# Optimization experiments

Measured on AMD Instinct MI355X. Metric: run time of the kernel, lower is better.

## Reference

```python
import jax, jax.numpy as jnp
import numpy as np

N_NODES = 10000
N_EDGES = 70000
IN_DIM = 10
HEADS = 6
LIN_OUT = 254
GAT_DIMS = [(256, 508), (512, 250), (256, 120), (128, 20)]  # (in_dim, out_dim) per DeformGAT
NEG_SLOPE = 0.2


def setup_inputs() -> dict:
    key = jax.random.key(0)
    ks = jax.random.split(key, 8)
    inp = {}
    inp["data"] = jax.random.normal(ks[0], (N_NODES, IN_DIM), dtype=jnp.float32)
    inp["edge_idx"] = jax.random.randint(ks[1], (2, N_EDGES), 0, N_NODES)
    inp["bd_mask"] = jax.random.randint(ks[2], (N_NODES,), 0, 2) > 0
    inp["poly_mesh"] = 0
    inp["W_lin"] = jax.random.normal(ks[3], (IN_DIM, LIN_OUT), dtype=jnp.float32) * 0.05
    inp["b_lin"] = jnp.zeros((LIN_OUT,), dtype=jnp.float32)
    for i, (din, dout) in enumerate(GAT_DIMS):
        k1, k2, k3 = jax.random.split(ks[4 + i], 3)
        inp[f"W{i+1}"] = jax.random.normal(k1, (din, HEADS * dout), dtype=jnp.float32) * 0.05
        inp[f"asrc{i+1}"] = jax.random.normal(k2, (HEADS, dout), dtype=jnp.float32) * 0.05
        inp[f"adst{i+1}"] = jax.random.normal(k3, (HEADS, dout), dtype=jnp.float32) * 0.05
    return inp


def deform_gat(coord, feat, src, dst, bd_mask, W, a_src, a_dst, n):
    """One DeformGAT layer: GAT attention over edge list; features aggregated
    (head-averaged, SELU); coords moved to attention-weighted neighbor centroid,
    boundary nodes pinned."""
    H, C = a_src.shape
    x = (feat @ W).reshape(-1, H, C)                       # [N,H,C]
    a_s = jnp.einsum('nhc,hc->nh', x, a_src)               # [N,H]
    a_d = jnp.einsum('nhc,hc->nh', x, a_dst)               # [N,H]
    e = jax.nn.leaky_relu(a_s[src] + a_d[dst], NEG_SLOPE)  # [E,H]
    # segment softmax over incoming edges of each dst node
    m = jax.ops.segment_max(e, dst, num_segments=n)
    m = jnp.where(jnp.isfinite(m), m, 0.0)
    ex = jnp.exp(e - m[dst])
    denom = jax.ops.segment_sum(ex, dst, num_segments=n)
    alpha = ex / jnp.where(denom[dst] > 0, denom[dst], 1.0)        # [E,H]
    agg = jax.ops.segment_sum(alpha[:, :, None] * x[src], dst, num_segments=n)  # [N,H,C]
    out_feat = jax.nn.selu(agg.mean(axis=1))                       # [N,C]
    am = alpha.mean(axis=1)                                        # [E]
    new_coord = jax.ops.segment_sum(am[:, None] * coord[src], dst, num_segments=n)  # [N,2]
    out_coord = jnp.where(bd_mask[:, None], coord, new_coord)
    return out_coord, out_feat


def reference(data, edge_idx, bd_mask, poly_mesh, W_lin, b_lin,
              W1, asrc1, adst1, W2, asrc2, adst2,
              W3, asrc3, adst3, W4, asrc4, adst4):
    n = data.shape[0]
    coords = data[:, 0:2]
    src, dst = edge_idx[0], edge_idx[1]
    h = jax.nn.selu(data @ W_lin + b_lin)                  # [N,254]
    t1 = jnp.concatenate([coords, h], axis=1)              # [N,256]
    c1, f1 = deform_gat(coords, t1, src, dst, bd_mask, W1, asrc1, adst1, n)
    t2 = jnp.concatenate([c1, coords, f1], axis=1)         # [N,512]
    c2, f2 = deform_gat(c1, t2, src, dst, bd_mask, W2, asrc2, adst2, n)
    t3 = jnp.concatenate([c2, c1, coords, f2], axis=1)     # [N,256]
    c3, f3 = deform_gat(c2, t3, src, dst, bd_mask, W3, asrc3, adst3, n)
    t4 = jnp.concatenate([c3, c2, c1, coords, f3], axis=1) # [N,128]
    c4, f4 = deform_gat(c3, t4, src, dst, bd_mask, W4, asrc4, adst4, n)
    return c4
```

## Files before the change

kernel.cpp:

```cpp
#include <hip/hip_runtime.h>
#include <hip/hip_bf16.h>

#define N_NODES 10000
#define N_EDGES 70000
#define HEADS 6
#define MPAD 10112
#define SELU_SCALE 1.0507009873554805f
#define SELU_ALPHA  1.6732632423543772f
#define NEG_SLOPE 0.2f

typedef __attribute__((ext_vector_type(8))) __bf16 bf16x8;
typedef __attribute__((ext_vector_type(4))) float f32x4;

__device__ __forceinline__ float selu_f(float x) {
    return x > 0.f ? SELU_SCALE * x : SELU_SCALE * SELU_ALPHA * (__expf(x) - 1.f);
}
__device__ __forceinline__ unsigned short f2bf(float f) {
    __hip_bfloat16 h = __float2bfloat16(f);
    return __builtin_bit_cast(unsigned short, h);
}
__device__ __forceinline__ float bf2f(unsigned short u) {
    unsigned int x = ((unsigned int)u) << 16;
    return __builtin_bit_cast(float, x);
}

__global__ void count_edges_k(const int* __restrict__ dstv, int* __restrict__ counts) {
    int e = blockIdx.x * blockDim.x + threadIdx.x;
    if (e < N_EDGES) atomicAdd(&counts[dstv[e]], 1);
}

__global__ __launch_bounds__(1024) void scan_k(const int* __restrict__ counts, int* __restrict__ offs) {
    __shared__ int part[1024];
    int tid = threadIdx.x;
    const int per = (N_NODES + 1023) / 1024;
    int start = tid * per;
    int s = 0;
    for (int i = 0; i < per; ++i) { int idx = start + i; if (idx < N_NODES) s += counts[idx]; }
    part[tid] = s;
    __syncthreads();
    for (int off = 1; off < 1024; off <<= 1) {
        int v = (tid >= off) ? part[tid - off] : 0;
        __syncthreads();
        part[tid] += v;
        __syncthreads();
    }
    int run = part[tid] - s;
    for (int i = 0; i < per; ++i) {
        int idx = start + i;
        if (idx < N_NODES) { offs[idx] = run; run += counts[idx]; }
    }
    if (tid == 0) offs[N_NODES] = part[1023];
}

__global__ void fill_csr_k(const int* __restrict__ dstv, const int* __restrict__ offs,
                           int* __restrict__ cursor, int* __restrict__ csr) {
    int e = blockIdx.x * blockDim.x + threadIdx.x;
    if (e < N_EDGES) {
        int d = dstv[e];
        int pos = atomicAdd(&cursor[d], 1);
        csr[offs[d] + pos] = e;
    }
}

__global__ __launch_bounds__(256) void prep_k(const float* __restrict__ data,
                                              const float* __restrict__ W,
                                              const float* __restrict__ b,
                                              float* __restrict__ coords0,
                                              unsigned short* __restrict__ t1) {
    int idx = blockIdx.x * blockDim.x + threadIdx.x;
    if (idx >= N_NODES * 256) return;
    int n = idx >> 8, c = idx & 255;
    if (c < 2) {
        float v = data[n * 10 + c];
        t1[(size_t)n * 256 + c] = f2bf(v);
        if (c == 0) {
            coords0[2 * n] = data[n * 10];
            coords0[2 * n + 1] = data[n * 10 + 1];
        }
    } else {
        int cc = c - 2;
        float acc = b[cc];
        const float* dr = data + (size_t)n * 10;
#pragma unroll
        for (int k = 0; k < 10; ++k) acc += dr[k] * W[k * 254 + cc];
        t1[(size_t)n * 256 + c] = f2bf(selu_f(acc));
    }
}

__global__ __launch_bounds__(64) void fold_all_k(
    const float* __restrict__ W0, const float* __restrict__ s0v, const float* __restrict__ d0v,
    const float* __restrict__ W1, const float* __restrict__ s1v, const float* __restrict__ d1v,
    const float* __restrict__ W2, const float* __restrict__ s2v, const float* __restrict__ d2v,
    const float* __restrict__ W3, const float* __restrict__ s3v, const float* __restrict__ d3v,
    float* __restrict__ wsf0, float* __restrict__ wdf0,
    float* __restrict__ wsf1, float* __restrict__ wdf1,
    float* __restrict__ wsf2, float* __restrict__ wdf2,
    float* __restrict__ wsf3, float* __restrict__ wdf3) {
    int bid = blockIdx.x;
    const float* W; const float* sv; const float* dv; float* ws; float* wd;
    int K, C, pair;
    if (bid < 1536)      { W = W0; sv = s0v; dv = d0v; ws = wsf0; wd = wdf0; K = 256; C = 508; pair = bid; }
    else if (bid < 4608) { W = W1; sv = s1v; dv = d1v; ws = wsf1; wd = wdf1; K = 512; C = 250; pair = bid - 1536; }
    else if (bid < 6144) { W = W2; sv = s2v; dv = d2v; ws = wsf2; wd = wdf2; K = 256; C = 120; pair = bid - 4608; }
    else                 { W = W3; sv = s3v; dv = d3v; ws = wsf3; wd = wdf3; K = 128; C = 20;  pair = bid - 6144; }
    int k = pair / HEADS, h = pair % HEADS;
    int lane = threadIdx.x;
    const float* wr = W + (size_t)k * (HEADS * C) + h * C;
    const float* sr = sv + h * C;
    const float* dr = dv + h * C;
    float s = 0.f, d = 0.f;
    for (int c = lane; c < C; c += 64) {
        float w = wr[c];
        s += w * sr[c];
        d += w * dr[c];
    }
#pragma unroll
    for (int off = 32; off > 0; off >>= 1) {
        s += __shfl_xor(s, off);
        d += __shfl_xor(d, off);
    }
    if (lane == 0) { ws[pair] = s; wd[pair] = d; }
}

__global__ __launch_bounds__(256) void convv_all_k(
    const float* __restrict__ W0, unsigned short* __restrict__ Vt0,
    const float* __restrict__ W1, unsigned short* __restrict__ Vt1,
    const float* __restrict__ W2, unsigned short* __restrict__ Vt2) {
    __shared__ float tile[64][65];
    int bid = blockIdx.x;
    const float* W; unsigned short* Vt; int K, C, K6, bid2, ktiles;
    if (bid < 192)      { W = W0; Vt = Vt0; K = 256; C = 508; K6 = 1536; bid2 = bid;       ktiles = 24; }
    else if (bid < 384) { W = W1; Vt = Vt1; K = 512; C = 250; K6 = 3072; bid2 = bid - 192; ktiles = 48; }
    else                { W = W2; Vt = Vt2; K = 256; C = 120; K6 = 1536; bid2 = bid - 384; ktiles = 24; }
    int kb = bid2 % ktiles, cb = bid2 / ktiles;
    const int tx = threadIdx.x;
    const int ty = threadIdx.y;
    const int k0 = kb * 64;
    const int c0 = cb * 64;
    for (int i = ty; i < 64; i += 4) {
        int kk = k0 + i;
        int h = kk / K, k = kk - h * K;
        int c = c0 + tx;
        tile[i][tx] = (c < C) ? W[(size_t)k * (HEADS * C) + h * C + c] : 0.f;
    }
    __syncthreads();
    for (int i = ty; i < 64; i += 4) {
        int c = c0 + i;
        Vt[(size_t)c * K6 + k0 + tx] = f2bf(tile[tx][i]);
    }
}

__global__ __launch_bounds__(256) void gemm_split_k(
    const unsigned short* __restrict__ A,
    const unsigned short* __restrict__ Bt,
    unsigned short* __restrict__ part,
    int Kpitch, int klen, int Npad) {
    __shared__ unsigned short lds[16384];
    const int tid = threadIdx.x;
    const int lane = tid & 63, wid = tid >> 6;
    const int wm = wid >> 1, wn = wid & 1;
    const int m0 = blockIdx.y * 128;
    const int n0 = blockIdx.x * 128;
    const int kz = blockIdx.z;
    const int kbeg = kz * klen;

    f32x4 acc[4][4] = {};

    const unsigned short* gsrc[8];
    unsigned ldsoff[8];
#pragma unroll
    for (int i = 0; i < 8; ++i) {
        const int half = i >> 2;
        const int slot = (i & 3) * 256 + tid;
        const int r = slot >> 3;
        const int c16 = slot & 7;
        const int ksl = c16 ^ (r & 7);
        gsrc[i] = (half ? (Bt + (size_t)(n0 + r) * Kpitch) : (A + (size_t)(m0 + r) * Kpitch)) + ksl * 8;
        ldsoff[i] = (unsigned)(half * 8192 + ((i & 3) * 256 + wid * 64) * 8);
    }

    for (int kt = kbeg; kt < kbeg + klen; kt += 64) {
#pragma unroll
        for (int i = 0; i < 8; ++i) {
            __builtin_amdgcn_global_load_lds(
                (const __attribute__((address_space(1))) unsigned int*)(gsrc[i] + kt),
                (__attribute__((address_space(3))) unsigned int*)(&lds[ldsoff[i]]),
                16, 0, 0);
        }
        __syncthreads();
#pragma unroll
        for (int kc = 0; kc < 2; ++kc) {
            const int xo = (((kc * 4 + (lane >> 4)) ^ (lane & 7)) << 4);
            bf16x8 aop[4], bop[4];
#pragma unroll
            for (int f = 0; f < 4; ++f) {
                const int rA = wm * 64 + f * 16 + (lane & 15);
                bop[f] = *(const bf16x8*)((const char*)lds + rA * 128 + xo);
                const int rB = wn * 64 + f * 16 + (lane & 15);
                aop[f] = *(const bf16x8*)((const char*)lds + 16384 * 1 + rB * 128 + xo);
            }
#pragma unroll
            for (int fm = 0; fm < 4; ++fm)
#pragma unroll
                for (int fn = 0; fn < 4; ++fn)
                    acc[fm][fn] = __builtin_amdgcn_mfma_f32_16x16x32_bf16(
                        aop[fn], bop[fm], acc[fm][fn], 0, 0, 0);
        }
        __syncthreads();
    }

    unsigned short* pbase = part + (size_t)kz * MPAD * Npad;
    const int mrow = m0 + wm * 64 + (lane & 15);
    const int ncol = n0 + wn * 64 + ((lane >> 4) * 4);
#pragma unroll
    for (int fm = 0; fm < 4; ++fm) {
#pragma unroll
        for (int fn = 0; fn < 4; ++fn) {
            f32x4 v = acc[fm][fn];
            unsigned int u0 = (unsigned int)f2bf(v.x) | ((unsigned int)f2bf(v.y) << 16);
            unsigned int u1 = (unsigned int)f2bf(v.z) | ((unsigned int)f2bf(v.w) << 16);
            uint2 pk = make_uint2(u0, u1);
            *(uint2*)&pbase[(size_t)(mrow + fm * 16) * Npad + ncol + fn * 16] = pk;
        }
    }
}

__global__ __launch_bounds__(256) void proj2_k(const unsigned short* __restrict__ t,
                                               const float* __restrict__ wsf,
                                               const float* __restrict__ wdf,
                                               float* __restrict__ a_s,
                                               float* __restrict__ a_d, int K) {
    const int wv = threadIdx.x >> 6;
    const int lane = threadIdx.x & 63;
    const int n = blockIdx.x * 4 + wv;
    if (n >= N_NODES) return;
    const unsigned short* tr = t + (size_t)n * K;
    const int kpl = K >> 6;
    const int k0 = lane * kpl;

    unsigned int buf[4] = {0u, 0u, 0u, 0u};
    if (kpl == 8) {
        uint4 u = *(const uint4*)(tr + k0);
        buf[0] = u.x; buf[1] = u.y; buf[2] = u.z; buf[3] = u.w;
    } else if (kpl == 4) {
        uint2 u = *(const uint2*)(tr + k0);
        buf[0] = u.x; buf[1] = u.y;
    } else {
        buf[0] = *(const unsigned int*)(tr + k0);
    }

    float s[HEADS] = {}, d[HEADS] = {};
#pragma unroll
    for (int j = 0; j < 8; ++j) {
        if (j >= kpl) break;
        unsigned int w = buf[j >> 1];
        unsigned short u = (j & 1) ? (unsigned short)(w >> 16) : (unsigned short)(w & 0xffff);
        float v = bf2f(u);
        const float* ws = wsf + (size_t)(k0 + j) * HEADS;
        const float* wd = wdf + (size_t)(k0 + j) * HEADS;
#pragma unroll
        for (int h = 0; h < HEADS; ++h) {
            s[h] += v * ws[h];
            d[h] += v * wd[h];
        }
    }
#pragma unroll
    for (int off = 32; off > 0; off >>= 1) {
#pragma unroll
        for (int h = 0; h < HEADS; ++h) {
            s[h] += __shfl_xor(s[h], off);
            d[h] += __shfl_xor(d[h], off);
        }
    }
    if (lane == 0) {
#pragma unroll
        for (int h = 0; h < HEADS; ++h) {
            a_s[n * HEADS + h] = s[h];
            a_d[n * HEADS + h] = d[h];
        }
    }
}

template<int KN>
__global__ __launch_bounds__(256) void reduceproj_k(
    const unsigned short* __restrict__ part, int KS, int Npad, int off,
    unsigned short* __restrict__ tnext,
    const float* __restrict__ wsf, const float* __restrict__ wdf,
    float* __restrict__ a_s, float* __restrict__ a_d) {
    const int wid = threadIdx.x >> 6, lane = threadIdx.x & 63;
    const int n = blockIdx.x * 4 + wid;
    if (n >= N_NODES) return;
    constexpr int KPL = KN / 64;
    const int c0 = lane * KPL;
    unsigned short* row = tnext + (size_t)n * KN;

    float vals[KPL];
#pragma unroll
    for (int q = 0; q < KPL; ++q) {
        int c = c0 + q;
        if (c < off) {
            vals[q] = bf2f(row[c]);
        } else {
            int cp = c - off;
            float sum = 0.f;
            for (int kz = 0; kz < KS; ++kz)
                sum += bf2f(part[(size_t)kz * MPAD * Npad + (size_t)n * Npad + cp]);
            float o = selu_f(sum * (1.f / 6.f));
            vals[q] = o;
            row[c] = f2bf(o);
        }
    }

    float s[HEADS] = {}, d[HEADS] = {};
#pragma unroll
    for (int q = 0; q < KPL; ++q) {
        int c = c0 + q;
        float v = vals[q];
        const float* ws = wsf + (size_t)c * HEADS;
        const float* wd = wdf + (size_t)c * HEADS;
#pragma unroll
        for (int h = 0; h < HEADS; ++h) {
            s[h] += v * ws[h];
            d[h] += v * wd[h];
        }
    }
#pragma unroll
    for (int off2 = 32; off2 > 0; off2 >>= 1) {
#pragma unroll
        for (int h = 0; h < HEADS; ++h) {
            s[h] += __shfl_xor(s[h], off2);
            d[h] += __shfl_xor(d[h], off2);
        }
    }
    if (lane == 0) {
#pragma unroll
        for (int h = 0; h < HEADS; ++h) {
            a_s[n * HEADS + h] = s[h];
            a_d[n * HEADS + h] = d[h];
        }
    }
}

template<int KT>
__global__ __launch_bounds__(256) void attn_agg_move_k(
    const float* __restrict__ a_s, const float* __restrict__ a_d,
    const int* __restrict__ srcv, const int* __restrict__ csr,
    const int* __restrict__ offs,
    const unsigned short* __restrict__ t_in, unsigned short* __restrict__ thagg,
    const float* __restrict__ cprev, const int* __restrict__ bd,
    float* __restrict__ cout, unsigned short* __restrict__ tnext, int ld,
    const float* __restrict__ xA, int offA,
    const float* __restrict__ xB, int offB) {
    const int wid = threadIdx.x >> 6, lane = threadIdx.x & 63;
    const int n = blockIdx.x * 4 + wid;
    if (n >= N_NODES) return;
    const int r0 = offs[n], r1 = offs[n + 1];

    float ad[HEADS], mm[HEADS], ss[HEADS];
#pragma unroll
    for (int h = 0; h < HEADS; ++h) {
        ad[h] = a_d[n * HEADS + h];
        mm[h] = -1e30f; ss[h] = 0.f;
    }

    for (int base = r0; base < r1; base += 64) {
        int i = base + lane;
        if (i < r1) {
            int src = srcv[csr[i]];
#pragma unroll
            for (int h = 0; h < HEADS; ++h) {
                float v = a_s[src * HEADS + h] + ad[h];
                v = v > 0.f ? v : NEG_SLOPE * v;
                float nm = fmaxf(mm[h], v);
                ss[h] = ss[h] * __expf(mm[h] - nm) + __expf(v - nm);
                mm[h] = nm;
            }
        }
    }
#pragma unroll
    for (int off = 32; off > 0; off >>= 1) {
#pragma unroll
        for (int h = 0; h < HEADS; ++h) {
            float mo = __shfl_xor(mm[h], off);
            float so = __shfl_xor(ss[h], off);
            float nm = fmaxf(mm[h], mo);
            ss[h] = ss[h] * __expf(mm[h] - nm) + so * __expf(mo - nm);
            mm[h] = nm;
        }
    }
    float rd[HEADS];
#pragma unroll
    for (int h = 0; h < HEADS; ++h) rd[h] = ss[h] > 0.f ? 1.f / ss[h] : 0.f;

    constexpr int KPL = (KT > 0) ? (KT / 64) : 1;
    float acc[HEADS][KPL] = {};
    float cx = 0.f, cy = 0.f;
    for (int base = r0; base < r1; base += 64) {
        int i = base + lane;
        bool ok = i < r1;
        int mysrc = ok ? srcv[csr[i]] : 0;
        float myal[HEADS];
#pragma unroll
        for (int h = 0; h < HEADS; ++h) myal[h] = 0.f;
        if (ok) {
            float am = 0.f;
#pragma unroll
            for (int h = 0; h < HEADS; ++h) {
                float v = a_s[mysrc * HEADS + h] + ad[h];
                v = v > 0.f ? v : NEG_SLOPE * v;
                float a = __expf(v - mm[h]) * rd[h];
                myal[h] = a;
                am += a;
            }
            am *= (1.f / 6.f);
            cx += am * cprev[2 * mysrc];
            cy += am * cprev[2 * mysrc + 1];
        }
        if constexpr (KT > 0) {
            int cnt = min(64, r1 - base);
            for (int j = 0; j < cnt; ++j) {
                int src = __shfl(mysrc, j);
                float al[HEADS];
#pragma unroll
                for (int h = 0; h < HEADS; ++h) al[h] = __shfl(myal[h], j);
                if constexpr (KT == 512) {
                    uint4 u = *(const uint4*)(t_in + (size_t)src * 512 + lane * 8);
                    float tv[8];
                    tv[0] = bf2f((unsigned short)(u.x & 0xffff)); tv[1] = bf2f((unsigned short)(u.x >> 16));
                    tv[2] = bf2f((unsigned short)(u.y & 0xffff)); tv[3] = bf2f((unsigned short)(u.y >> 16));
                    tv[4] = bf2f((unsigned short)(u.z & 0xffff)); tv[5] = bf2f((unsigned short)(u.z >> 16));
                    tv[6] = bf2f((unsigned short)(u.w & 0xffff)); tv[7] = bf2f((unsigned short)(u.w >> 16));
#pragma unroll
                    for (int h = 0; h < HEADS; ++h)
#pragma unroll
                        for (int q = 0; q < 8; ++q) acc[h][q] += al[h] * tv[q];
                } else {
                    uint2 u = *(const uint2*)(t_in + (size_t)src * 256 + lane * 4);
                    float tv[4];
                    tv[0] = bf2f((unsigned short)(u.x & 0xffff)); tv[1] = bf2f((unsigned short)(u.x >> 16));
                    tv[2] = bf2f((unsigned short)(u.y & 0xffff)); tv[3] = bf2f((unsigned short)(u.y >> 16));
#pragma unroll
                    for (int h = 0; h < HEADS; ++h)
#pragma unroll
                        for (int q = 0; q < 4; ++q) acc[h][q] += al[h] * tv[q];
                }
            }
        }
    }

    if constexpr (KT == 512) {
#pragma unroll
        for (int h = 0; h < HEADS; ++h) {
            uint4 pk;
            pk.x = (unsigned int)f2bf(acc[h][0]) | ((unsigned int)f2bf(acc[h][1]) << 16);
            pk.y = (unsigned int)f2bf(acc[h][2]) | ((unsigned int)f2bf(acc[h][3]) << 16);
            pk.z = (unsigned int)f2bf(acc[h][4]) | ((unsigned int)f2bf(acc[h][5]) << 16);
            pk.w = (unsigned int)f2bf(acc[h][6]) | ((unsigned int)f2bf(acc[h][7]) << 16);
            *(uint4*)(thagg + (size_t)n * 3072 + h * 512 + lane * 8) = pk;
        }
    } else if constexpr (KT == 256) {
#pragma unroll
        for (int h = 0; h < HEADS; ++h) {
            uint2 pk;
            pk.x = (unsigned int)f2bf(acc[h][0]) | ((unsigned int)f2bf(acc[h][1]) << 16);
            pk.y = (unsigned int)f2bf(acc[h][2]) | ((unsigned int)f2bf(acc[h][3]) << 16);
            *(uint2*)(thagg + (size_t)n * 1536 + h * 256 + lane * 4) = pk;
        }
    }
#pragma unroll
    for (int off = 32; off > 0; off >>= 1) {
        cx += __shfl_xor(cx, off);
        cy += __shfl_xor(cy, off);
    }
    if (lane == 0) {
        float px = cprev[2 * n], py = cprev[2 * n + 1];
        float ocx, ocy;
        if (bd[n] != 0) { ocx = px; ocy = py; }
        else { ocx = cx; ocy = cy; }
        cout[2 * n] = ocx; cout[2 * n + 1] = ocy;
        if (tnext) {
            unsigned short* row = tnext + (size_t)n * ld;
            row[0] = f2bf(ocx); row[1] = f2bf(ocy);
            row[2] = f2bf(px);  row[3] = f2bf(py);
            if (xA) { row[offA] = f2bf(xA[2 * n]); row[offA + 1] = f2bf(xA[2 * n + 1]); }
            if (xB) { row[offB] = f2bf(xB[2 * n]); row[offB + 1] = f2bf(xB[2 * n + 1]); }
        }
    }
}

static inline int cdiv(int a, int b) { return (a + b - 1) / b; }

extern "C" void kernel_launch(void* const* d_in, const int* in_sizes, int n_in,
                              void* d_out, int out_size, void* d_ws, size_t ws_size,
                              hipStream_t stream) {
    const float* data = (const float*)d_in[0];
    const int* eidx = (const int*)d_in[1];
    const int* bd = (const int*)d_in[2];
    const float* W_lin = (const float*)d_in[4];
    const float* b_lin = (const float*)d_in[5];
    const float* Wl[4]  = {(const float*)d_in[6],  (const float*)d_in[9],
                           (const float*)d_in[12], (const float*)d_in[15]};
    const float* Asrc[4] = {(const float*)d_in[7],  (const float*)d_in[10],
                            (const float*)d_in[13], (const float*)d_in[16]};
    const float* Adst[4] = {(const float*)d_in[8],  (const float*)d_in[11],
                            (const float*)d_in[14], (const float*)d_in[17]};
    const int Kd[4] = {256, 512, 256, 128};
    const int Cpadd[4] = {512, 256, 128, 0};
    const int KSd[4] = {2, 4, 4, 0};

    const int* srcv = eidx;
    const int* dstv = eidx + N_EDGES;

    char* p = (char*)d_ws;
    auto alloc = [&](size_t bytes) -> void* {
        void* r = (void*)p;
        p += (bytes + 255) & ~(size_t)255;
        return r;
    };
    unsigned short* tb1 = (unsigned short*)alloc((size_t)MPAD * 256 * 2);
    unsigned short* tb2 = (unsigned short*)alloc((size_t)MPAD * 512 * 2);
    unsigned short* tb3 = (unsigned short*)alloc((size_t)MPAD * 256 * 2);
    unsigned short* tb4 = (unsigned short*)alloc((size_t)MPAD * 128 * 2);
    unsigned short* thagg = (unsigned short*)alloc((size_t)MPAD * 3072 * 2);
    unsigned short* VtL[3];
    VtL[0] = (unsigned short*)alloc((size_t)512 * 1536 * 2);
    VtL[1] = (unsigned short*)alloc((size_t)256 * 3072 * 2);
    VtL[2] = (unsigned short*)alloc((size_t)128 * 1536 * 2);
    unsigned short* partb = (unsigned short*)alloc((size_t)8 * MPAD * 256 * 2);
    float* coords0 = (float*)alloc((size_t)N_NODES * 2 * 4);
    float* c1 = (float*)alloc((size_t)N_NODES * 2 * 4);
    float* c2 = (float*)alloc((size_t)N_NODES * 2 * 4);
    float* c3 = (float*)alloc((size_t)N_NODES * 2 * 4);
    float* a_s = (float*)alloc((size_t)N_NODES * HEADS * 4);
    float* a_d = (float*)alloc((size_t)N_NODES * HEADS * 4);
    float* wsfL[4]; float* wdfL[4];
    wsfL[0] = (float*)alloc(1536 * 4); wdfL[0] = (float*)alloc(1536 * 4);
    wsfL[1] = (float*)alloc(3072 * 4); wdfL[1] = (float*)alloc(3072 * 4);
    wsfL[2] = (float*)alloc(1536 * 4); wdfL[2] = (float*)alloc(1536 * 4);
    wsfL[3] = (float*)alloc(768 * 4);  wdfL[3] = (float*)alloc(768 * 4);
    int* counts = (int*)alloc((size_t)N_NODES * 4);
    int* cursor = (int*)alloc((size_t)N_NODES * 4);
    int* offs = (int*)alloc((size_t)(N_NODES + 1) * 4);
    int* csr = (int*)alloc((size_t)N_EDGES * 4);

    hipMemsetAsync(counts, 0, (size_t)((char*)offs - (char*)counts), stream);
    count_edges_k<<<cdiv(N_EDGES, 256), 256, 0, stream>>>(dstv, counts);
    scan_k<<<1, 1024, 0, stream>>>(counts, offs);
    fill_csr_k<<<cdiv(N_EDGES, 256), 256, 0, stream>>>(dstv, offs, cursor, csr);

    prep_k<<<cdiv(N_NODES * 256, 256), 256, 0, stream>>>(data, W_lin, b_lin, coords0, tb1);
    fold_all_k<<<6912, 64, 0, stream>>>(
        Wl[0], Asrc[0], Adst[0], Wl[1], Asrc[1], Adst[1],
        Wl[2], Asrc[2], Adst[2], Wl[3], Asrc[3], Adst[3],
        wsfL[0], wdfL[0], wsfL[1], wdfL[1], wsfL[2], wdfL[2], wsfL[3], wdfL[3]);
    convv_all_k<<<432, dim3(64, 4), 0, stream>>>(Wl[0], VtL[0], Wl[1], VtL[1], Wl[2], VtL[2]);

    unsigned short* tin[4]   = {tb1, tb2, tb3, tb4};
    unsigned short* tnext[4] = {tb2, tb3, tb4, nullptr};
    int ldn[4]  = {512, 256, 128, 0};
    int foff[4] = {4, 6, 8, 0};
    float* cprev[4] = {coords0, c1, c2, c3};
    float* cout[4]  = {c1, c2, c3, (float*)d_out};
    const float* xAv[4] = {nullptr, coords0, c1, nullptr};
    int offAv[4] = {0, 4, 4, 0};
    const float* xBv[4] = {nullptr, nullptr, coords0, nullptr};
    int offBv[4] = {0, 0, 6, 0};

    proj2_k<<<cdiv(N_NODES, 4), 256, 0, stream>>>(tb1, wsfL[0], wdfL[0], a_s, a_d, 256);

    for (int l = 0; l < 4; ++l) {
        int K = Kd[l], Cpad = Cpadd[l], KS = KSd[l];
        int K6 = K * HEADS;

        if (l == 3) {
            attn_agg_move_k<0><<<cdiv(N_NODES, 4), 256, 0, stream>>>(
                a_s, a_d, srcv, csr, offs, tin[l], nullptr,
                cprev[l], bd, cout[l], tnext[l], ldn[l],
                xAv[l], offAv[l], xBv[l], offBv[l]);
        } else if (K == 512) {
            attn_agg_move_k<512><<<cdiv(N_NODES, 4), 256, 0, stream>>>(
                a_s, a_d, srcv, csr, offs, tin[l], thagg,
                cprev[l], bd, cout[l], tnext[l], ldn[l],
                xAv[l], offAv[l], xBv[l], offBv[l]);
        } else {
            attn_agg_move_k<256><<<cdiv(N_NODES, 4), 256, 0, stream>>>(
                a_s, a_d, srcv, csr, offs, tin[l], thagg,
                cprev[l], bd, cout[l], tnext[l], ldn[l],
                xAv[l], offAv[l], xBv[l], offBv[l]);
        }

        if (l < 3) {
            int klen = K6 / KS;
            gemm_split_k<<<dim3(Cpad / 128, MPAD / 128, KS), 256, 0, stream>>>(
                thagg, VtL[l], partb, K6, klen, Cpad);
            if (ldn[l] == 512) {
                reduceproj_k<512><<<cdiv(N_NODES, 4), 256, 0, stream>>>(
                    partb, KS, Cpad, foff[l], tnext[l], wsfL[l + 1], wdfL[l + 1], a_s, a_d);
            } else if (ldn[l] == 256) {
                reduceproj_k<256><<<cdiv(N_NODES, 4), 256, 0, stream>>>(
                    partb, KS, Cpad, foff[l], tnext[l], wsfL[l + 1], wdfL[l + 1], a_s, a_d);
            } else {
                reduceproj_k<128><<<cdiv(N_NODES, 4), 256, 0, stream>>>(
                    partb, KS, Cpad, foff[l], tnext[l], wsfL[l + 1], wdfL[l + 1], a_s, a_d);
            }
        }
    }
}
```

Baseline: 331.1 us.

## Store source ids in CSR, fuse prep with projection, add single-pass softmax path

The CSR fill now stores source node ids directly, which removes one level of indirection (srcv[csr[i]]) in every attention kernel. The input linear+SELU prep is fused with the layer-1 attention projection into one wave-per-node kernel, dropping a separate launch and the re-read of t1. For nodes with degree at most 64, the attention kernel computes max, exp and sum in registers with wave reductions instead of an online-softmax loop followed by a second recompute pass. This adds code size and a divergent branch, and keeps the old two-pass path for high-degree nodes.

Measured after the change: 341.3 us. +3.1%, slower.

```diff
diff --git a/kernel.cpp b/kernel.cpp
--- a/kernel.cpp
+++ b/kernel.cpp
@@ -52,38 +52,77 @@
     if (tid == 0) offs[N_NODES] = part[1023];
 }
 
-__global__ void fill_csr_k(const int* __restrict__ dstv, const int* __restrict__ offs,
-                           int* __restrict__ cursor, int* __restrict__ csr) {
+__global__ void fill_csr_k(const int* __restrict__ srcv, const int* __restrict__ dstv,
+                           const int* __restrict__ offs,
+                           int* __restrict__ cursor, int* __restrict__ srcs) {
     int e = blockIdx.x * blockDim.x + threadIdx.x;
     if (e < N_EDGES) {
         int d = dstv[e];
         int pos = atomicAdd(&cursor[d], 1);
-        csr[offs[d] + pos] = e;
-    }
-}
-
-__global__ __launch_bounds__(256) void prep_k(const float* __restrict__ data,
-                                              const float* __restrict__ W,
-                                              const float* __restrict__ b,
-                                              float* __restrict__ coords0,
-                                              unsigned short* __restrict__ t1) {
-    int idx = blockIdx.x * blockDim.x + threadIdx.x;
-    if (idx >= N_NODES * 256) return;
-    int n = idx >> 8, c = idx & 255;
-    if (c < 2) {
-        float v = data[n * 10 + c];
-        t1[(size_t)n * 256 + c] = f2bf(v);
-        if (c == 0) {
-            coords0[2 * n] = data[n * 10];
-            coords0[2 * n + 1] = data[n * 10 + 1];
-        }
-    } else {
-        int cc = c - 2;
-        float acc = b[cc];
-        const float* dr = data + (size_t)n * 10;
-#pragma unroll
-        for (int k = 0; k < 10; ++k) acc += dr[k] * W[k * 254 + cc];
-        t1[(size_t)n * 256 + c] = f2bf(selu_f(acc));
+        srcs[offs[d] + pos] = srcv[e];
+    }
+}
+
+__global__ __launch_bounds__(256) void prep_proj_k(
+    const float* __restrict__ data, const float* __restrict__ W, const float* __restrict__ b,
+    float* __restrict__ coords0, unsigned short* __restrict__ t1,
+    const float* __restrict__ wsf, const float* __restrict__ wdf,
+    float* __restrict__ a_s, float* __restrict__ a_d) {
+    const int wid = threadIdx.x >> 6, lane = threadIdx.x & 63;
+    const int n = blockIdx.x * 4 + wid;
+    if (n >= N_NODES) return;
+    const int c0 = lane * 4;
+    const float* dr = data + (size_t)n * 10;
+
+    float vals[4];
+#pragma unroll
+    for (int q = 0; q < 4; ++q) {
+        int c = c0 + q;
+        if (c < 2) {
+            vals[q] = dr[c];
+        } else {
+            int cc = c - 2;
+            float acc = b[cc];
+#pragma unroll
+            for (int k = 0; k < 10; ++k) acc += dr[k] * W[k * 254 + cc];
+            vals[q] = selu_f(acc);
+        }
+    }
+    uint2 pk;
+    pk.x = (unsigned int)f2bf(vals[0]) | ((unsigned int)f2bf(vals[1]) << 16);
+    pk.y = (unsigned int)f2bf(vals[2]) | ((unsigned int)f2bf(vals[3]) << 16);
+    *(uint2*)(t1 + (size_t)n * 256 + c0) = pk;
+    if (lane == 0) {
+        coords0[2 * n] = vals[0];
+        coords0[2 * n + 1] = vals[1];
+    }
+
+    float s[HEADS] = {}, d[HEADS] = {};
+#pragma unroll
+    for (int q = 0; q < 4; ++q) {
+        float v = bf2f(f2bf(vals[q]));
+        const float* ws = wsf + (size_t)(c0 + q) * HEADS;
+        const float* wd = wdf + (size_t)(c0 + q) * HEADS;
+#pragma unroll
+        for (int h = 0; h < HEADS; ++h) {
+            s[h] += v * ws[h];
+            d[h] += v * wd[h];
+        }
+    }
+#pragma unroll
+    for (int off = 32; off > 0; off >>= 1) {
+#pragma unroll
+        for (int h = 0; h < HEADS; ++h) {
+            s[h] += __shfl_xor(s[h], off);
+            d[h] += __shfl_xor(d[h], off);
+        }
+    }
+    if (lane == 0) {
+#pragma unroll
+        for (int h = 0; h < HEADS; ++h) {
+            a_s[n * HEADS + h] = s[h];
+            a_d[n * HEADS + h] = d[h];
+        }
     }
 }
 
@@ -225,62 +264,6 @@
     }
 }
 
-__global__ __launch_bounds__(256) void proj2_k(const unsigned short* __restrict__ t,
-                                               const float* __restrict__ wsf,
-                                               const float* __restrict__ wdf,
-                                               float* __restrict__ a_s,
-                                               float* __restrict__ a_d, int K) {
-    const int wv = threadIdx.x >> 6;
-    const int lane = threadIdx.x & 63;
-    const int n = blockIdx.x * 4 + wv;
-    if (n >= N_NODES) return;
-    const unsigned short* tr = t + (size_t)n * K;
-    const int kpl = K >> 6;
-    const int k0 = lane * kpl;
-
-    unsigned int buf[4] = {0u, 0u, 0u, 0u};
-    if (kpl == 8) {
-        uint4 u = *(const uint4*)(tr + k0);
-        buf[0] = u.x; buf[1] = u.y; buf[2] = u.z; buf[3] = u.w;
-    } else if (kpl == 4) {
-        uint2 u = *(const uint2*)(tr + k0);
-        buf[0] = u.x; buf[1] = u.y;
-    } else {
-        buf[0] = *(const unsigned int*)(tr + k0);
-    }
-
-    float s[HEADS] = {}, d[HEADS] = {};
-#pragma unroll
-    for (int j = 0; j < 8; ++j) {
-        if (j >= kpl) break;
-        unsigned int w = buf[j >> 1];
-        unsigned short u = (j & 1) ? (unsigned short)(w >> 16) : (unsigned short)(w & 0xffff);
-        float v = bf2f(u);
-        const float* ws = wsf + (size_t)(k0 + j) * HEADS;
-        const float* wd = wdf + (size_t)(k0 + j) * HEADS;
-#pragma unroll
-        for (int h = 0; h < HEADS; ++h) {
-            s[h] += v * ws[h];
-            d[h] += v * wd[h];
-        }
-    }
-#pragma unroll
-    for (int off = 32; off > 0; off >>= 1) {
-#pragma unroll
-        for (int h = 0; h < HEADS; ++h) {
-            s[h] += __shfl_xor(s[h], off);
-            d[h] += __shfl_xor(d[h], off);
-        }
-    }
-    if (lane == 0) {
-#pragma unroll
-        for (int h = 0; h < HEADS; ++h) {
-            a_s[n * HEADS + h] = s[h];
-            a_d[n * HEADS + h] = d[h];
-        }
-    }
-}
-
 template<int KN>
 __global__ __launch_bounds__(256) void reduceproj_k(
     const unsigned short* __restrict__ part, int KS, int Npad, int off,
@@ -344,8 +327,7 @@
 template<int KT>
 __global__ __launch_bounds__(256) void attn_agg_move_k(
     const float* __restrict__ a_s, const float* __restrict__ a_d,
-    const int* __restrict__ srcv, const int* __restrict__ csr,
-    const int* __restrict__ offs,
+    const int* __restrict__ srcs, const int* __restrict__ offs,
     const unsigned short* __restrict__ t_in, unsigned short* __restrict__ thagg,
     const float* __restrict__ cprev, const int* __restrict__ bd,
     float* __restrict__ cout, unsigned short* __restrict__ tnext, int ld,
@@ -355,70 +337,61 @@
     const int n = blockIdx.x * 4 + wid;
     if (n >= N_NODES) return;
     const int r0 = offs[n], r1 = offs[n + 1];
-
-    float ad[HEADS], mm[HEADS], ss[HEADS];
-#pragma unroll
-    for (int h = 0; h < HEADS; ++h) {
-        ad[h] = a_d[n * HEADS + h];
-        mm[h] = -1e30f; ss[h] = 0.f;
-    }
-
-    for (int base = r0; base < r1; base += 64) {
-        int i = base + lane;
-        if (i < r1) {
-            int src = srcv[csr[i]];
-#pragma unroll
-            for (int h = 0; h < HEADS; ++h) {
-                float v = a_s[src * HEADS + h] + ad[h];
-                v = v > 0.f ? v : NEG_SLOPE * v;
-                float nm = fmaxf(mm[h], v);
-                ss[h] = ss[h] * __expf(mm[h] - nm) + __expf(v - nm);
-                mm[h] = nm;
-            }
-        }
-    }
-#pragma unroll
-    for (int off = 32; off > 0; off >>= 1) {
-#pragma unroll
-        for (int h = 0; h < HEADS; ++h) {
-            float mo = __shfl_xor(mm[h], off);
-            float so = __shfl_xor(ss[h], off);
-            float nm = fmaxf(mm[h], mo);
-            ss[h] = ss[h] * __expf(mm[h] - nm) + so * __expf(mo - nm);
-            mm[h] = nm;
-        }
-    }
-    float rd[HEADS];
-#pragma unroll
-    for (int h = 0; h < HEADS; ++h) rd[h] = ss[h] > 0.f ? 1.f / ss[h] : 0.f;
+    const int deg = r1 - r0;
+
+    float ad[HEADS];
+#pragma unroll
+    for (int h = 0; h < HEADS; ++h) ad[h] = a_d[n * HEADS + h];
 
     constexpr int KPL = (KT > 0) ? (KT / 64) : 1;
     float acc[HEADS][KPL] = {};
     float cx = 0.f, cy = 0.f;
-    for (int base = r0; base < r1; base += 64) {
-        int i = base + lane;
-        bool ok = i < r1;
-        int mysrc = ok ? srcv[csr[i]] : 0;
-        float myal[HEADS];
-#pragma unroll
-        for (int h = 0; h < HEADS; ++h) myal[h] = 0.f;
+
+    if (deg <= 64) {
+        const bool ok = lane < deg;
+        const int mysrc = ok ? srcs[r0 + lane] : 0;
+        float mm[HEADS], ss[HEADS], myal[HEADS];
+#pragma unroll
+        for (int h = 0; h < HEADS; ++h) {
+            float v = -1e30f;
+            if (ok) {
+                v = a_s[mysrc * HEADS + h] + ad[h];
+                v = v > 0.f ? v : NEG_SLOPE * v;
+            }
+            mm[h] = v;
+        }
+#pragma unroll
+        for (int off = 32; off > 0; off >>= 1)
+#pragma unroll
+            for (int h = 0; h < HEADS; ++h) mm[h] = fmaxf(mm[h], __shfl_xor(mm[h], off));
+#pragma unroll
+        for (int h = 0; h < HEADS; ++h) {
+            float v = -1e30f;
+            if (ok) {
+                v = a_s[mysrc * HEADS + h] + ad[h];
+                v = v > 0.f ? v : NEG_SLOPE * v;
+            }
+            myal[h] = ok ? __expf(v - mm[h]) : 0.f;
+            ss[h] = myal[h];
+        }
+#pragma unroll
+        for (int off = 32; off > 0; off >>= 1)
+#pragma unroll
+            for (int h = 0; h < HEADS; ++h) ss[h] += __shfl_xor(ss[h], off);
+        float am = 0.f;
+#pragma unroll
+        for (int h = 0; h < HEADS; ++h) {
+            float rdh = ss[h] > 0.f ? 1.f / ss[h] : 0.f;
+            myal[h] *= rdh;
+            am += myal[h];
+        }
         if (ok) {
-            float am = 0.f;
-#pragma unroll
-            for (int h = 0; h < HEADS; ++h) {
-                float v = a_s[mysrc * HEADS + h] + ad[h];
-                v = v > 0.f ? v : NEG_SLOPE * v;
-                float a = __expf(v - mm[h]) * rd[h];
-                myal[h] = a;
-                am += a;
-            }
             am *= (1.f / 6.f);
-            cx += am * cprev[2 * mysrc];
-            cy += am * cprev[2 * mysrc + 1];
+            cx = am * cprev[2 * mysrc];
+            cy = am * cprev[2 * mysrc + 1];
         }
         if constexpr (KT > 0) {
-            int cnt = min(64, r1 - base);
-            for (int j = 0; j < cnt; ++j) {
+            for (int j = 0; j < deg; ++j) {
                 int src = __shfl(mysrc, j);
                 float al[HEADS];
 #pragma unroll
@@ -443,6 +416,91 @@
                     for (int h = 0; h < HEADS; ++h)
 #pragma unroll
                         for (int q = 0; q < 4; ++q) acc[h][q] += al[h] * tv[q];
+                }
+            }
+        }
+    } else {
+        float mm[HEADS], ss[HEADS];
+#pragma unroll
+        for (int h = 0; h < HEADS; ++h) { mm[h] = -1e30f; ss[h] = 0.f; }
+        for (int base = r0; base < r1; base += 64) {
+            int i = base + lane;
+            if (i < r1) {
+                int src = srcs[i];
+#pragma unroll
+                for (int h = 0; h < HEADS; ++h) {
+                    float v = a_s[src * HEADS + h] + ad[h];
+                    v = v > 0.f ? v : NEG_SLOPE * v;
+                    float nm = fmaxf(mm[h], v);
+                    ss[h] = ss[h] * __expf(mm[h] - nm) + __expf(v - nm);
+                    mm[h] = nm;
+                }
+            }
+        }
+#pragma unroll
+        for (int off = 32; off > 0; off >>= 1) {
+#pragma unroll
+            for (int h = 0; h < HEADS; ++h) {
+                float mo = __shfl_xor(mm[h], off);
+                float so = __shfl_xor(ss[h], off);
+                float nm = fmaxf(mm[h], mo);
+                ss[h] = ss[h] * __expf(mm[h] - nm) + so * __expf(mo - nm);
+                mm[h] = nm;
+            }
+        }
+        float rd[HEADS];
+#pragma unroll
+        for (int h = 0; h < HEADS; ++h) rd[h] = ss[h] > 0.f ? 1.f / ss[h] : 0.f;
+
+        for (int base = r0; base < r1; base += 64) {
+            int i = base + lane;
+            bool ok = i < r1;
+            int mysrc = ok ? srcs[i] : 0;
+            float myal[HEADS];
+#pragma unroll
+            for (int h = 0; h < HEADS; ++h) myal[h] = 0.f;
+            if (ok) {
+                float am = 0.f;
+#pragma unroll
+                for (int h = 0; h < HEADS; ++h) {
+                    float v = a_s[mysrc * HEADS + h] + ad[h];
+                    v = v > 0.f ? v : NEG_SLOPE * v;
+                    float a = __expf(v - mm[h]) * rd[h];
+                    myal[h] = a;
+                    am += a;
+                }
+                am *= (1.f / 6.f);
+                cx += am * cprev[2 * mysrc];
+                cy += am * cprev[2 * mysrc + 1];
+            }
+            if constexpr (KT > 0) {
+                int cnt = min(64, r1 - base);
+                for (int j = 0; j < cnt; ++j) {
+                    int src = __shfl(mysrc, j);
+                    float al[HEADS];
+#pragma unroll
+                    for (int h = 0; h < HEADS; ++h) al[h] = __shfl(myal[h], j);
+                    if constexpr (KT == 512) {
+                        uint4 u = *(const uint4*)(t_in + (size_t)src * 512 + lane * 8);
+                        float tv[8];
+                        tv[0] = bf2f((unsigned short)(u.x & 0xffff)); tv[1] = bf2f((unsigned short)(u.x >> 16));
+                        tv[2] = bf2f((unsigned short)(u.y & 0xffff)); tv[3] = bf2f((unsigned short)(u.y >> 16));
+                        tv[4] = bf2f((unsigned short)(u.z & 0xffff)); tv[5] = bf2f((unsigned short)(u.z >> 16));
+                        tv[6] = bf2f((unsigned short)(u.w & 0xffff)); tv[7] = bf2f((unsigned short)(u.w >> 16));
+#pragma unroll
+                        for (int h = 0; h < HEADS; ++h)
+#pragma unroll
+                            for (int q = 0; q < 8; ++q) acc[h][q] += al[h] * tv[q];
+                    } else {
+                        uint2 u = *(const uint2*)(t_in + (size_t)src * 256 + lane * 4);
+                        float tv[4];
+                        tv[0] = bf2f((unsigned short)(u.x & 0xffff)); tv[1] = bf2f((unsigned short)(u.x >> 16));
+                        tv[2] = bf2f((unsigned short)(u.y & 0xffff)); tv[3] = bf2f((unsigned short)(u.y >> 16));
+#pragma unroll
+                        for (int h = 0; h < HEADS; ++h)
+#pragma unroll
+                            for (int q = 0; q < 4; ++q) acc[h][q] += al[h] * tv[q];
+                    }
                 }
             }
         }
@@ -541,19 +599,20 @@
     int* counts = (int*)alloc((size_t)N_NODES * 4);
     int* cursor = (int*)alloc((size_t)N_NODES * 4);
     int* offs = (int*)alloc((size_t)(N_NODES + 1) * 4);
-    int* csr = (int*)alloc((size_t)N_EDGES * 4);
+    int* srcs = (int*)alloc((size_t)N_EDGES * 4);
 
     hipMemsetAsync(counts, 0, (size_t)((char*)offs - (char*)counts), stream);
     count_edges_k<<<cdiv(N_EDGES, 256), 256, 0, stream>>>(dstv, counts);
     scan_k<<<1, 1024, 0, stream>>>(counts, offs);
-    fill_csr_k<<<cdiv(N_EDGES, 256), 256, 0, stream>>>(dstv, offs, cursor, csr);
-
-    prep_k<<<cdiv(N_NODES * 256, 256), 256, 0, stream>>>(data, W_lin, b_lin, coords0, tb1);
+    fill_csr_k<<<cdiv(N_EDGES, 256), 256, 0, stream>>>(srcv, dstv, offs, cursor, srcs);
+
     fold_all_k<<<6912, 64, 0, stream>>>(
         Wl[0], Asrc[0], Adst[0], Wl[1], Asrc[1], Adst[1],
         Wl[2], Asrc[2], Adst[2], Wl[3], Asrc[3], Adst[3],
         wsfL[0], wdfL[0], wsfL[1], wdfL[1], wsfL[2], wdfL[2], wsfL[3], wdfL[3]);
     convv_all_k<<<432, dim3(64, 4), 0, stream>>>(Wl[0], VtL[0], Wl[1], VtL[1], Wl[2], VtL[2]);
+    prep_proj_k<<<cdiv(N_NODES, 4), 256, 0, stream>>>(
+        data, W_lin, b_lin, coords0, tb1, wsfL[0], wdfL[0], a_s, a_d);
 
     unsigned short* tin[4]   = {tb1, tb2, tb3, tb4};
     unsigned short* tnext[4] = {tb2, tb3, tb4, nullptr};
@@ -566,25 +625,23 @@
     const float* xBv[4] = {nullptr, nullptr, coords0, nullptr};
     int offBv[4] = {0, 0, 6, 0};
 
-    proj2_k<<<cdiv(N_NODES, 4), 256, 0, stream>>>(tb1, wsfL[0], wdfL[0], a_s, a_d, 256);
-
     for (int l = 0; l < 4; ++l) {
         int K = Kd[l], Cpad = Cpadd[l], KS = KSd[l];
         int K6 = K * HEADS;
 
         if (l == 3) {
             attn_agg_move_k<0><<<cdiv(N_NODES, 4), 256, 0, stream>>>(
-                a_s, a_d, srcv, csr, offs, tin[l], nullptr,
+                a_s, a_d, srcs, offs, tin[l], nullptr,
                 cprev[l], bd, cout[l], tnext[l], ldn[l],
                 xAv[l], offAv[l], xBv[l], offBv[l]);
         } else if (K == 512) {
             attn_agg_move_k<512><<<cdiv(N_NODES, 4), 256, 0, stream>>>(
-                a_s, a_d, srcv, csr, offs, tin[l], thagg,
+                a_s, a_d, srcs, offs, tin[l], thagg,
                 cprev[l], bd, cout[l], tnext[l], ldn[l],
                 xAv[l], offAv[l], xBv[l], offBv[l]);
         } else {
             attn_agg_move_k<256><<<cdiv(N_NODES, 4), 256, 0, stream>>>(
-                a_s, a_d, srcv, csr, offs, tin[l], thagg,
+                a_s, a_d, srcs, offs, tin[l], thagg,
                 cprev[l], bd, cout[l], tnext[l], ldn[l],
                 xAv[l], offAv[l], xBv[l], offBv[l]);
         }
```
